# Kernel optimization log

Hardware: AMD Instinct MI355X
Metric: run time of the kernel (lower is better)

## Reference

```python
import jax, jax.numpy as jnp
import numpy as np

NUM_LAYER = 5
EMB = 256
N = 100000
E = 300000
SELF_LOOP_BOND = 4
BN_EPS = 1e-5


def setup_inputs() -> dict:
    key = jax.random.key(0)
    ks = jax.random.split(key, 16)
    f = lambda k, shape: jax.random.normal(k, shape, jnp.float32) * 0.02
    return {
        "x_atom": jax.random.randint(ks[0], (N,), 0, 120),
        "x_chir": jax.random.randint(ks[1], (N,), 0, 3),
        "edge_index": jax.random.randint(ks[2], (2, E), 0, N),
        "edge_bond": jax.random.randint(ks[3], (E,), 0, 4),
        "edge_dir": jax.random.randint(ks[4], (E,), 0, 3),
        "atom_emb": f(ks[5], (120, EMB)),
        "chir_emb": f(ks[6], (3, EMB)),
        "bond_embs": f(ks[7], (NUM_LAYER, 6, EMB)),
        "dir_embs": f(ks[8], (NUM_LAYER, 3, EMB)),
        "W1s": f(ks[9], (NUM_LAYER, 2 * EMB, EMB)),
        "b1s": f(ks[10], (NUM_LAYER, 2 * EMB)),
        "W2s": f(ks[11], (NUM_LAYER, EMB, 2 * EMB)),
        "b2s": f(ks[12], (NUM_LAYER, EMB)),
        "bn_w": jnp.ones((NUM_LAYER, EMB), jnp.float32),
        "bn_b": jnp.zeros((NUM_LAYER, EMB), jnp.float32),
    }


def reference(x_atom, x_chir, edge_index, edge_bond, edge_dir,
              atom_emb, chir_emb, bond_embs, dir_embs,
              W1s, b1s, W2s, b2s, bn_w, bn_b):
    n = x_atom.shape[0]
    src, dst = edge_index[0], edge_index[1]
    # add self loops (edge_attr = [4, 0] for each node)
    loop = jnp.arange(n)
    src_full = jnp.concatenate([src, loop])          # [E+N]
    dst_full = jnp.concatenate([dst, loop])          # [E+N]
    bond_full = jnp.concatenate([edge_bond, jnp.full((n,), SELF_LOOP_BOND, edge_bond.dtype)])
    dir_full = jnp.concatenate([edge_dir, jnp.zeros((n,), edge_dir.dtype)])

    # initial node features: atom + chirality embeddings
    h = atom_emb[x_atom] + chir_emb[x_chir]          # [N, EMB]

    for l in range(NUM_LAYER):
        # per-layer edge embeddings (bond type + bond direction)
        e_emb = bond_embs[l][bond_full] + dir_embs[l][dir_full]   # [E+N, EMB]
        # message = x_j + edge_attr; aggregate = scatter-add to dst
        msg = h[src_full] + e_emb                                  # gather
        agg = jax.ops.segment_sum(msg, dst_full, num_segments=n)  # scatter-add
        # update MLP: Linear(EMB->2EMB) -> ReLU -> Linear(2EMB->EMB)
        hmid = jax.nn.relu(agg @ W1s[l].T + b1s[l])                # [N, 2EMB]
        h2 = hmid @ W2s[l].T + b2s[l]                              # [N, EMB]
        # batch norm (training mode: batch statistics, biased variance)
        mean = h2.mean(axis=0)
        var = h2.var(axis=0)
        h2 = (h2 - mean) * jax.lax.rsqrt(var + BN_EPS) * bn_w[l] + bn_b[l]
        # relu on all but last layer; dropout with p=0 is identity
        if l < NUM_LAYER - 1:
            h2 = jax.nn.relu(h2)
        h = h2
    # JK == 'last'
    return h
```

## Files before the change

### kernel.cpp

```cpp
#include <hip/hip_runtime.h>

#define EMB 256
#define NLAYER 5
#define CHUNK 1024

typedef unsigned int u32;
typedef unsigned short u16;

typedef __bf16 bf16x8 __attribute__((ext_vector_type(8)));
typedef float f32x4 __attribute__((ext_vector_type(4)));

__device__ __forceinline__ float bf2f(u16 u) {
    union { u32 i; float f; } x; x.i = ((u32)u) << 16; return x.f;
}
__device__ __forceinline__ u16 f2bf(float f) {
    union { float f; u32 i; } x; x.f = f;
    u32 r = x.i + 0x7FFFu + ((x.i >> 16) & 1u);
    return (u16)(r >> 16);
}
__device__ __forceinline__ void unpack4(uint2 p, float* o) {
    union { u32 i; float f; } a, b, c, d;
    a.i = p.x << 16; b.i = p.x & 0xFFFF0000u;
    c.i = p.y << 16; d.i = p.y & 0xFFFF0000u;
    o[0] = a.f; o[1] = b.f; o[2] = c.f; o[3] = d.f;
}

__global__ void k_detect(const u32* __restrict__ bnw_raw, int* __restrict__ flag) {
    if (threadIdx.x == 0 && blockIdx.x == 0)
        *flag = (bnw_raw[0] == 0x3F803F80u) ? 1 : 0;
}

struct Cvt { const void* s; u16* d; int n; };
struct CvtTab { Cvt t[10]; };

__global__ void k_convert(CvtTab tab, const int* __restrict__ flag, int maxn) {
    int f = *flag;
    int stride = gridDim.x * blockDim.x;
    for (int i = blockIdx.x * blockDim.x + threadIdx.x; i < maxn; i += stride) {
        for (int j = 0; j < 10; j++) {
            if (i < tab.t[j].n) {
                u16 v;
                if (f) v = ((const u16*)tab.t[j].s)[i];
                else   v = f2bf(((const float*)tab.t[j].s)[i]);
                tab.t[j].d[i] = v;
            }
        }
    }
}

__global__ void k_zero(u32* p, int n) {
    int i = blockIdx.x * blockDim.x + threadIdx.x;
    if (i < n) p[i] = 0u;
}

__global__ void k_hist(const int* __restrict__ eidx, const int* __restrict__ ebond,
                       const int* __restrict__ edir,
                       u32* __restrict__ cnt, u32* __restrict__ cntb, u32* __restrict__ cntd, int E) {
    int e = blockIdx.x * blockDim.x + threadIdx.x;
    if (e >= E) return;
    int dst = eidx[E + e];
    atomicAdd(&cnt[dst], 1u);
    atomicAdd(&cntb[dst * 4 + ebond[e]], 1u);
    atomicAdd(&cntd[dst * 3 + edir[e]], 1u);
}

__global__ void k_chunksum(const u32* __restrict__ cnt, u32* __restrict__ partial, int N) {
    int b = blockIdx.x, t = threadIdx.x;
    int base = b * CHUNK + t * 4;
    u32 s = 0;
    for (int i = 0; i < 4; i++) { int idx = base + i; if (idx < N) s += cnt[idx]; }
    __shared__ u32 red[256];
    red[t] = s; __syncthreads();
    for (int o = 128; o > 0; o >>= 1) { if (t < o) red[t] += red[t + o]; __syncthreads(); }
    if (t == 0) partial[b] = red[0];
}

__global__ void k_scanpartial(u32* partial, u32* indptr, int nch, int N) {
    if (threadIdx.x == 0 && blockIdx.x == 0) {
        u32 run = 0;
        for (int i = 0; i < nch; i++) { u32 x = partial[i]; partial[i] = run; run += x; }
        indptr[N] = run;
    }
}

__global__ void k_chunkscan(const u32* __restrict__ cnt, const u32* __restrict__ partial,
                            u32* __restrict__ indptr, u32* __restrict__ fillp, int N) {
    int b = blockIdx.x, t = threadIdx.x;
    int base = b * CHUNK + t * 4;
    u32 c[4]; u32 tsum = 0;
    for (int i = 0; i < 4; i++) { int idx = base + i; c[i] = (idx < N) ? cnt[idx] : 0u; tsum += c[i]; }
    __shared__ u32 sc[256];
    sc[t] = tsum; __syncthreads();
    for (int o = 1; o < 256; o <<= 1) {
        u32 x = (t >= o) ? sc[t - o] : 0u;
        __syncthreads();
        sc[t] += x;
        __syncthreads();
    }
    u32 run = partial[b] + sc[t] - tsum;
    for (int i = 0; i < 4; i++) {
        int idx = base + i;
        if (idx < N) { indptr[idx] = run; fillp[idx] = run; }
        run += c[i];
    }
}

__global__ void k_fill(const int* __restrict__ eidx, u32* __restrict__ fillp,
                       u32* __restrict__ srcs, int E) {
    int e = blockIdx.x * blockDim.x + threadIdx.x;
    if (e >= E) return;
    int dst = eidx[E + e];
    u32 pos = atomicAdd(&fillp[dst], 1u);
    srcs[pos] = (u32)eidx[e];
}

__global__ void k_h0(const int* __restrict__ xa, const int* __restrict__ xc,
                     const u16* __restrict__ aemb, const u16* __restrict__ cemb,
                     u16* __restrict__ H, int N) {
    int wave = threadIdx.x >> 6, lane = threadIdx.x & 63;
    int v = blockIdx.x * 4 + wave;
    if (v >= N) return;
    int a = xa[v], c = xc[v];
    int c4 = lane * 4;
    uint2 pa = *(const uint2*)(aemb + (size_t)a * EMB + c4);
    uint2 pc = *(const uint2*)(cemb + (size_t)c * EMB + c4);
    float fa[4], fc[4];
    unpack4(pa, fa); unpack4(pc, fc);
    ushort4 ov;
    ov.x = f2bf(fa[0] + fc[0]); ov.y = f2bf(fa[1] + fc[1]);
    ov.z = f2bf(fa[2] + fc[2]); ov.w = f2bf(fa[3] + fc[3]);
    *(ushort4*)(H + (size_t)v * EMB + c4) = ov;
}

__global__ void k_scatter(const u16* __restrict__ H, const u32* __restrict__ indptr,
                          const u32* __restrict__ srcs,
                          const u32* __restrict__ cntb, const u32* __restrict__ cntd,
                          const u16* __restrict__ bemb, const u16* __restrict__ demb,
                          const float* __restrict__ scsh, int relu,
                          u16* __restrict__ AGG, int N) {
    int wave = threadIdx.x >> 6, lane = threadIdx.x & 63;
    int v = blockIdx.x * 4 + wave;
    if (v >= N) return;
    int c4 = lane * 4;
    float sc[4] = {1.f, 1.f, 1.f, 1.f}, sh[4] = {0.f, 0.f, 0.f, 0.f};
    if (scsh) {
        float4 s0 = *(const float4*)(scsh + c4);
        float4 s1 = *(const float4*)(scsh + 256 + c4);
        sc[0] = s0.x; sc[1] = s0.y; sc[2] = s0.z; sc[3] = s0.w;
        sh[0] = s1.x; sh[1] = s1.y; sh[2] = s1.z; sh[3] = s1.w;
    }
    float acc[4] = {0.f, 0.f, 0.f, 0.f};
    u32 beg = indptr[v], end = indptr[v + 1];
    for (u32 e = beg; e < end; e++) {
        u32 s = srcs[e];
        uint2 p = *(const uint2*)(H + (size_t)s * EMB + c4);
        float f[4]; unpack4(p, f);
        for (int i = 0; i < 4; i++) {
            float y = f[i] * sc[i] + sh[i];
            if (relu) y = fmaxf(y, 0.f);
            acc[i] += y;
        }
    }
    {
        uint2 p = *(const uint2*)(H + (size_t)v * EMB + c4);
        float f[4]; unpack4(p, f);
        for (int i = 0; i < 4; i++) {
            float y = f[i] * sc[i] + sh[i];
            if (relu) y = fmaxf(y, 0.f);
            acc[i] += y;
        }
    }
    float cb[5];
    cb[0] = (float)cntb[v * 4 + 0]; cb[1] = (float)cntb[v * 4 + 1];
    cb[2] = (float)cntb[v * 4 + 2]; cb[3] = (float)cntb[v * 4 + 3]; cb[4] = 1.f;
    float cd[3];
    cd[0] = (float)cntd[v * 3 + 0] + 1.f; cd[1] = (float)cntd[v * 3 + 1]; cd[2] = (float)cntd[v * 3 + 2];
    for (int b = 0; b < 5; b++) {
        uint2 p = *(const uint2*)(bemb + b * EMB + c4);
        float f[4]; unpack4(p, f);
        for (int i = 0; i < 4; i++) acc[i] += cb[b] * f[i];
    }
    for (int d = 0; d < 3; d++) {
        uint2 p = *(const uint2*)(demb + d * EMB + c4);
        float f[4]; unpack4(p, f);
        for (int i = 0; i < 4; i++) acc[i] += cd[d] * f[i];
    }
    ushort4 ov;
    ov.x = f2bf(acc[0]); ov.y = f2bf(acc[1]); ov.z = f2bf(acc[2]); ov.w = f2bf(acc[3]);
    *(ushort4*)(AGG + (size_t)v * EMB + c4) = ov;
}

#define KP 264

__global__ __launch_bounds__(256, 2) void k_fused(
    const u16* __restrict__ A, const u16* __restrict__ W1, const u16* __restrict__ b1,
    const u16* __restrict__ W2, const u16* __restrict__ b2,
    u16* __restrict__ C, float* __restrict__ S, int M) {
    __shared__ __align__(16) u16 As[64 * KP];
    __shared__ __align__(16) u16 Hs[64 * KP];
    int m0 = blockIdx.x * 64;
    int t = threadIdx.x;
    int wave = t >> 6, lane = t & 63;
    int wn = wave * 64;
    int lr = lane & 15, quad = lane >> 4;

    for (int it = 0; it < 8; it++) {
        int ci = t + it * 256;
        int r = ci >> 5, kc = (ci & 31) * 8;
        int gr = m0 + r; if (gr > M - 1) gr = M - 1;
        *(uint4*)(As + r * KP + kc) = *(const uint4*)(A + (size_t)gr * 256 + kc);
    }

    f32x4 acc2[4][4];
    #pragma unroll
    for (int i = 0; i < 4; i++)
        #pragma unroll
        for (int j = 0; j < 4; j++)
            acc2[i][j] = (f32x4){0.f, 0.f, 0.f, 0.f};

    __syncthreads();

    #pragma unroll
    for (int nh = 0; nh < 2; nh++) {
        f32x4 acc1[4][4];
        #pragma unroll
        for (int i = 0; i < 4; i++)
            #pragma unroll
            for (int j = 0; j < 4; j++)
                acc1[i][j] = (f32x4){0.f, 0.f, 0.f, 0.f};
        const u16* W1h = W1 + (size_t)(nh * 256) * 256;
        #pragma unroll
        for (int ks = 0; ks < 256; ks += 32) {
            bf16x8 af[4], bfr[4];
            #pragma unroll
            for (int i = 0; i < 4; i++)
                af[i] = *(const bf16x8*)(As + (i * 16 + lr) * KP + ks + quad * 8);
            #pragma unroll
            for (int j = 0; j < 4; j++)
                bfr[j] = *(const bf16x8*)(W1h + (size_t)(wn + j * 16 + lr) * 256 + ks + quad * 8);
            #pragma unroll
            for (int i = 0; i < 4; i++)
                #pragma unroll
                for (int j = 0; j < 4; j++)
                    acc1[i][j] = __builtin_amdgcn_mfma_f32_16x16x32_bf16(af[i], bfr[j], acc1[i][j], 0, 0, 0);
        }
        __syncthreads();
        #pragma unroll
        for (int j = 0; j < 4; j++) {
            int hn = wn + j * 16 + lr;
            float bv = bf2f(b1[nh * 256 + hn]);
            #pragma unroll
            for (int i = 0; i < 4; i++)
                #pragma unroll
                for (int r = 0; r < 4; r++) {
                    float v = fmaxf(acc1[i][j][r] + bv, 0.f);
                    Hs[(i * 16 + quad * 4 + r) * KP + hn] = f2bf(v);
                }
        }
        __syncthreads();
        const u16* W2h = W2 + nh * 256;
        #pragma unroll
        for (int ks = 0; ks < 256; ks += 32) {
            bf16x8 af[4], bfr[4];
            #pragma unroll
            for (int i = 0; i < 4; i++)
                af[i] = *(const bf16x8*)(Hs + (i * 16 + lr) * KP + ks + quad * 8);
            #pragma unroll
            for (int j = 0; j < 4; j++)
                bfr[j] = *(const bf16x8*)(W2h + (size_t)(wn + j * 16 + lr) * 512 + ks + quad * 8);
            #pragma unroll
            for (int i = 0; i < 4; i++)
                #pragma unroll
                for (int j = 0; j < 4; j++)
                    acc2[i][j] = __builtin_amdgcn_mfma_f32_16x16x32_bf16(af[i], bfr[j], acc2[i][j], 0, 0, 0);
        }
    }

    #pragma unroll
    for (int j = 0; j < 4; j++) {
        int gn = wn + j * 16 + lr;
        float bv = bf2f(b2[gn]);
        float s = 0.f, q = 0.f;
        #pragma unroll
        for (int i = 0; i < 4; i++) {
            int mbase = m0 + i * 16 + quad * 4;
            #pragma unroll
            for (int r = 0; r < 4; r++) {
                int gm = mbase + r;
                if (gm < M) {
                    float v = acc2[i][j][r] + bv;
                    C[(size_t)gm * 256 + gn] = f2bf(v);
                    s += v; q += v * v;
                }
            }
        }
        s += __shfl_xor(s, 16, 64); s += __shfl_xor(s, 32, 64);
        q += __shfl_xor(q, 16, 64); q += __shfl_xor(q, 32, 64);
        if (quad == 0) {
            atomicAdd(&S[gn], s);
            atomicAdd(&S[256 + gn], q);
        }
    }
}

__global__ void k_finalize(const float* __restrict__ S, const u16* __restrict__ bnw,
                           const u16* __restrict__ bnb, float* __restrict__ scsh, float invN) {
    int c = threadIdx.x;
    float mean = S[c] * invN;
    float var = S[256 + c] * invN - mean * mean;
    var = fmaxf(var, 0.f);
    float inv = rsqrtf(var + 1e-5f);
    float sc = bf2f(bnw[c]) * inv;
    scsh[c] = sc;
    scsh[256 + c] = bf2f(bnb[c]) - mean * sc;
}

__global__ void k_out(const u16* __restrict__ H2, const float* __restrict__ scsh,
                      void* __restrict__ out, const int* __restrict__ flag, int N) {
    int wave = threadIdx.x >> 6, lane = threadIdx.x & 63;
    int v = blockIdx.x * 4 + wave;
    if (v >= N) return;
    int c4 = lane * 4;
    float4 s0 = *(const float4*)(scsh + c4);
    float4 s1 = *(const float4*)(scsh + 256 + c4);
    uint2 p = *(const uint2*)(H2 + (size_t)v * EMB + c4);
    float f[4]; unpack4(p, f);
    float o0 = f[0] * s0.x + s1.x;
    float o1 = f[1] * s0.y + s1.y;
    float o2 = f[2] * s0.z + s1.z;
    float o3 = f[3] * s0.w + s1.w;
    if (*flag) {
        ushort4 ov;
        ov.x = f2bf(o0); ov.y = f2bf(o1); ov.z = f2bf(o2); ov.w = f2bf(o3);
        *(ushort4*)((u16*)out + (size_t)v * EMB + c4) = ov;
    } else {
        float4 ov = make_float4(o0, o1, o2, o3);
        *(float4*)((float*)out + (size_t)v * EMB + c4) = ov;
    }
}

extern "C" void kernel_launch(void* const* d_in, const int* in_sizes, int n_in,
                              void* d_out, int out_size, void* d_ws, size_t ws_size,
                              hipStream_t stream) {
    const int* x_atom = (const int*)d_in[0];
    const int* x_chir = (const int*)d_in[1];
    const int* eidx   = (const int*)d_in[2];
    const int* ebond  = (const int*)d_in[3];
    const int* edir   = (const int*)d_in[4];

    const int N = in_sizes[0];
    const int E = in_sizes[3];

    char* p = (char*)d_ws;
    size_t off = 0;
    auto alloc = [&](size_t bytes) -> void* {
        void* r = p + off;
        off += bytes;
        off = (off + 255) & ~(size_t)255;
        return r;
    };
    u16* X   = (u16*)alloc((size_t)N * EMB * 2);
    u16* Y   = (u16*)alloc((size_t)N * EMB * 2);
    u32* cz  = (u32*)alloc(((size_t)8 * N + NLAYER * 512) * 4);
    u32* cnt  = cz;
    u32* cntb = cz + N;
    u32* cntd = cz + 5 * (size_t)N;
    float* stats5 = (float*)(cz + 8 * (size_t)N);
    u32* indptr = (u32*)alloc((size_t)(N + 1) * 4);
    u32* fillp  = (u32*)alloc((size_t)N * 4);
    u32* srcs   = (u32*)alloc((size_t)E * 4);
    u32* partial = (u32*)alloc(256 * 4);
    float* scsh  = (float*)alloc(512 * 4);
    int* flag    = (int*)alloc(256);

    int csz[10] = {120 * EMB, 3 * EMB, NLAYER * 6 * EMB, NLAYER * 3 * EMB,
                   NLAYER * 512 * EMB, NLAYER * 512, NLAYER * EMB * 512, NLAYER * EMB,
                   NLAYER * EMB, NLAYER * EMB};
    u16* cbuf[10];
    for (int j = 0; j < 10; j++) cbuf[j] = (u16*)alloc((size_t)csz[j] * 2);
    u16* atom_emb  = cbuf[0];
    u16* chir_emb  = cbuf[1];
    u16* bond_embs = cbuf[2];
    u16* dir_embs  = cbuf[3];
    u16* W1s = cbuf[4];
    u16* b1s = cbuf[5];
    u16* W2s = cbuf[6];
    u16* b2s = cbuf[7];
    u16* bnw = cbuf[8];
    u16* bnb = cbuf[9];

    const int nodeBlocks = (N + 3) / 4;
    const int nch = (N + CHUNK - 1) / CHUNK;

    k_detect<<<1, 64, 0, stream>>>((const u32*)d_in[13], flag);
    {
        CvtTab tab;
        int maxn = 0;
        for (int j = 0; j < 10; j++) {
            tab.t[j].s = d_in[5 + j];
            tab.t[j].d = cbuf[j];
            tab.t[j].n = csz[j];
            if (csz[j] > maxn) maxn = csz[j];
        }
        k_convert<<<(maxn + 255) / 256, 256, 0, stream>>>(tab, flag, maxn);
    }

    {
        int z = 8 * N + NLAYER * 512;
        k_zero<<<(z + 255) / 256, 256, 0, stream>>>(cz, z);
    }
    k_hist<<<(E + 255) / 256, 256, 0, stream>>>(eidx, ebond, edir, cnt, cntb, cntd, E);
    k_chunksum<<<nch, 256, 0, stream>>>(cnt, partial, N);
    k_scanpartial<<<1, 64, 0, stream>>>(partial, indptr, nch, N);
    k_chunkscan<<<nch, 256, 0, stream>>>(cnt, partial, indptr, fillp, N);
    k_fill<<<(E + 255) / 256, 256, 0, stream>>>(eidx, fillp, srcs, E);

    k_h0<<<nodeBlocks, 256, 0, stream>>>(x_atom, x_chir, atom_emb, chir_emb, X, N);

    u16* H = X;
    u16* A = Y;
    const int mT64 = (N + 63) / 64;
    for (int l = 0; l < NLAYER; l++) {
        const u16* bemb = bond_embs + (size_t)l * 6 * EMB;
        const u16* demb = dir_embs + (size_t)l * 3 * EMB;
        const u16* W1 = W1s + (size_t)l * 512 * EMB;
        const u16* B1 = b1s + (size_t)l * 512;
        const u16* W2 = W2s + (size_t)l * EMB * 512;
        const u16* B2 = b2s + (size_t)l * EMB;
        float* stats = stats5 + (size_t)l * 512;

        k_scatter<<<nodeBlocks, 256, 0, stream>>>(H, indptr, srcs, cntb, cntd, bemb, demb,
                                                  (l == 0) ? nullptr : scsh, (l == 0) ? 0 : 1,
                                                  A, N);
        k_fused<<<mT64, 256, 0, stream>>>(A, W1, B1, W2, B2, A, stats, N);
        k_finalize<<<1, 256, 0, stream>>>(stats, bnw + (size_t)l * EMB, bnb + (size_t)l * EMB,
                                          scsh, 1.0f / (float)N);
        u16* tmp = H; H = A; A = tmp;
    }

    k_out<<<nodeBlocks, 256, 0, stream>>>(H, scsh, d_out, flag, N);
}
```

Baseline: 1.316 ms.

## Split fused MLP hidden dim into four quarters to shrink LDS and raise occupancy

```diff
diff --git a/kernel.cpp b/kernel.cpp
--- a/kernel.cpp
+++ b/kernel.cpp
@@ -191,18 +191,20 @@
 }
 
 #define KP 264
-
-__global__ __launch_bounds__(256, 2) void k_fused(
+#define HS 136
+
+__global__ __launch_bounds__(256, 3) void k_fused(
     const u16* __restrict__ A, const u16* __restrict__ W1, const u16* __restrict__ b1,
     const u16* __restrict__ W2, const u16* __restrict__ b2,
     u16* __restrict__ C, float* __restrict__ S, int M) {
     __shared__ __align__(16) u16 As[64 * KP];
-    __shared__ __align__(16) u16 Hs[64 * KP];
+    __shared__ __align__(16) u16 Hs[64 * HS];
     int m0 = blockIdx.x * 64;
     int t = threadIdx.x;
     int wave = t >> 6, lane = t & 63;
+    int lr = lane & 15, quad = lane >> 4;
+    int wq = wave * 32;
     int wn = wave * 64;
-    int lr = lane & 15, quad = lane >> 4;
 
     for (int it = 0; it < 8; it++) {
         int ci = t + it * 256;
@@ -221,58 +223,61 @@
     __syncthreads();
 
     #pragma unroll
-    for (int nh = 0; nh < 2; nh++) {
-        f32x4 acc1[4][4];
+    for (int q = 0; q < 4; q++) {
+        f32x4 acc1[4][2];
         #pragma unroll
         for (int i = 0; i < 4; i++)
             #pragma unroll
-            for (int j = 0; j < 4; j++)
+            for (int j = 0; j < 2; j++)
                 acc1[i][j] = (f32x4){0.f, 0.f, 0.f, 0.f};
-        const u16* W1h = W1 + (size_t)(nh * 256) * 256;
+        const u16* W1q = W1 + (size_t)(q * 128) * 256;
         #pragma unroll
         for (int ks = 0; ks < 256; ks += 32) {
-            bf16x8 af[4], bfr[4];
+            bf16x8 af[4], wf[2];
             #pragma unroll
             for (int i = 0; i < 4; i++)
                 af[i] = *(const bf16x8*)(As + (i * 16 + lr) * KP + ks + quad * 8);
             #pragma unroll
+            for (int j = 0; j < 2; j++)
+                wf[j] = *(const bf16x8*)(W1q + (size_t)(wq + j * 16 + lr) * 256 + ks + quad * 8);
+            #pragma unroll
+            for (int j = 0; j < 2; j++)
+                #pragma unroll
+                for (int i = 0; i < 4; i++)
+                    acc1[i][j] = __builtin_amdgcn_mfma_f32_16x16x32_bf16(wf[j], af[i], acc1[i][j], 0, 0, 0);
+        }
+        __syncthreads();
+        #pragma unroll
+        for (int j = 0; j < 2; j++) {
+            int wl = wq + j * 16 + quad * 4;
+            ushort4 bq = *(const ushort4*)(b1 + q * 128 + wl);
+            float bv0 = bf2f(bq.x), bv1 = bf2f(bq.y), bv2 = bf2f(bq.z), bv3 = bf2f(bq.w);
+            #pragma unroll
+            for (int i = 0; i < 4; i++) {
+                ushort4 ov;
+                ov.x = f2bf(fmaxf(acc1[i][j][0] + bv0, 0.f));
+                ov.y = f2bf(fmaxf(acc1[i][j][1] + bv1, 0.f));
+                ov.z = f2bf(fmaxf(acc1[i][j][2] + bv2, 0.f));
+                ov.w = f2bf(fmaxf(acc1[i][j][3] + bv3, 0.f));
+                *(ushort4*)(Hs + (i * 16 + lr) * HS + wl) = ov;
+            }
+        }
+        __syncthreads();
+        const u16* W2q = W2 + q * 128;
+        #pragma unroll
+        for (int ks = 0; ks < 128; ks += 32) {
+            bf16x8 hf[4], vf[4];
+            #pragma unroll
+            for (int i = 0; i < 4; i++)
+                hf[i] = *(const bf16x8*)(Hs + (i * 16 + lr) * HS + ks + quad * 8);
+            #pragma unroll
             for (int j = 0; j < 4; j++)
-                bfr[j] = *(const bf16x8*)(W1h + (size_t)(wn + j * 16 + lr) * 256 + ks + quad * 8);
+                vf[j] = *(const bf16x8*)(W2q + (size_t)(wn + j * 16 + lr) * 512 + ks + quad * 8);
             #pragma unroll
             for (int i = 0; i < 4; i++)
                 #pragma unroll
                 for (int j = 0; j < 4; j++)
-                    acc1[i][j] = __builtin_amdgcn_mfma_f32_16x16x32_bf16(af[i], bfr[j], acc1[i][j], 0, 0, 0);
-        }
-        __syncthreads();
-        #pragma unroll
-        for (int j = 0; j < 4; j++) {
-            int hn = wn + j * 16 + lr;
-            float bv = bf2f(b1[nh * 256 + hn]);
-            #pragma unroll
-            for (int i = 0; i < 4; i++)
-                #pragma unroll
-                for (int r = 0; r < 4; r++) {
-                    float v = fmaxf(acc1[i][j][r] + bv, 0.f);
-                    Hs[(i * 16 + quad * 4 + r) * KP + hn] = f2bf(v);
-                }
-        }
-        __syncthreads();
-        const u16* W2h = W2 + nh * 256;
-        #pragma unroll
-        for (int ks = 0; ks < 256; ks += 32) {
-            bf16x8 af[4], bfr[4];
-            #pragma unroll
-            for (int i = 0; i < 4; i++)
-                af[i] = *(const bf16x8*)(Hs + (i * 16 + lr) * KP + ks + quad * 8);
-            #pragma unroll
-            for (int j = 0; j < 4; j++)
-                bfr[j] = *(const bf16x8*)(W2h + (size_t)(wn + j * 16 + lr) * 512 + ks + quad * 8);
-            #pragma unroll
-            for (int i = 0; i < 4; i++)
-                #pragma unroll
-                for (int j = 0; j < 4; j++)
-                    acc2[i][j] = __builtin_amdgcn_mfma_f32_16x16x32_bf16(af[i], bfr[j], acc2[i][j], 0, 0, 0);
+                    acc2[i][j] = __builtin_amdgcn_mfma_f32_16x16x32_bf16(hf[i], vf[j], acc2[i][j], 0, 0, 0);
         }
     }
 
```

After: 1.343 ms. 1.02x slower.
